# Performance work log

Hardware: AMD Instinct MI355X
Metric: run time of the kernel (lower is better)

Reference implementation:

```python
import jax, jax.numpy as jnp
import numpy as np

N = 100000
D = 512


def setup_inputs() -> dict:
    key = jax.random.key(0)
    k1, k2 = jax.random.split(key)
    features = jax.random.normal(k1, (N, D), dtype=jnp.float32)
    attn_w = jax.random.normal(k2, (D,), dtype=jnp.float32)
    attn_b = jnp.zeros((1,), dtype=jnp.float32)
    return {"features": features, "attn_w": attn_w, "attn_b": attn_b, "k": 4}


def reference(features, attn_w, attn_b, k):
    # features: [N, D]; sliding-window (half-width k, truncated at edges) mean
    n = features.shape[0]
    zero = jnp.zeros((1, features.shape[1]), dtype=features.dtype)
    cs = jnp.concatenate([zero, jnp.cumsum(features, axis=0)], axis=0)  # [N+1, D]
    i = jnp.arange(n)
    lo = jnp.maximum(i - k, 0)          # inclusive window start
    hi = jnp.minimum(i + k, n - 1)      # inclusive window end
    win_sum = cs[hi + 1] - cs[lo]       # [N, D]
    count = (hi - lo + 1).astype(features.dtype)[:, None]
    agg = win_sum / count               # [N, D] windowed means
    scores = agg @ attn_w + attn_b[0]   # [N]
    w = jax.nn.softmax(scores, axis=0)  # [N]
    bag = w @ agg                       # [D]
    return bag, w
```

## Files before the change

### kernel.cpp

```cpp
#include <hip/hip_runtime.h>
#include <math.h>

#define D 512
#define OWN 128
#define HALOA 8

__device__ __forceinline__ float dot4(float4 a, float4 b) {
    return a.x*b.x + a.y*b.y + a.z*b.z + a.w*b.w;
}

__global__ __launch_bounds__(256) void k_ab(
    const float* __restrict__ f, const float* __restrict__ w,
    const float* __restrict__ bptr, const int* __restrict__ kptr,
    float* __restrict__ e_out, float* __restrict__ psum,
    float* __restrict__ partial, int n)
{
    __shared__ float dots[OWN + 2 * HALOA];
    __shared__ float e_sh[OWN + 2 * HALOA];
    __shared__ float uu_sh[OWN];
    __shared__ float sm[4];
    int lane = threadIdx.x & 63;
    int wid  = threadIdx.x >> 6;
    int t    = threadIdx.x;
    int g0   = blockIdx.x * OWN - HALOA;

    const float4* wr = (const float4*)w;
    float4 b0 = wr[lane], b1 = wr[lane + 64];

    for (int lr = wid; lr < OWN + 2 * HALOA; lr += 4) {
        int row = g0 + lr;
        bool v = (row >= 0) && (row < n);
        const float4* fr = (const float4*)(f + (size_t)(v ? row : 0) * D);
        float4 a0 = fr[lane], a1 = fr[lane + 64];
        float s = dot4(a0, b0) + dot4(a1, b1);
        #pragma unroll
        for (int off = 32; off; off >>= 1) s += __shfl_down(s, off);
        if (lane == 0) dots[lr] = v ? s : 0.f;
    }
    __syncthreads();

    int k = *kptr;
    float bias = bptr[0];

    float e_reg = 0.f;
    if (t < OWN + 2 * HALOA) {
        int i = g0 + t;
        if (t >= HALOA - k && t < HALOA + OWN + k && i >= 0 && i < n) {
            int lo = max(i - k, 0), hi = min(i + k, n - 1);
            float s = 0.f;
            for (int q = lo; q <= hi; ++q) s += dots[q - g0];
            e_reg = __expf(s / (float)(hi - lo + 1) + bias);
        }
        e_sh[t] = e_reg;
    }
    __syncthreads();

    float pv = (t >= HALOA && t < HALOA + OWN) ? e_reg : 0.f;
    #pragma unroll
    for (int off = 32; off; off >>= 1) pv += __shfl_down(pv, off);
    if (lane == 0) sm[wid] = pv;
    __syncthreads();
    if (t == 0) psum[blockIdx.x] = sm[0] + sm[1] + sm[2] + sm[3];

    if (t < OWN) {
        int j = blockIdx.x * OWN + t;
        float acc = 0.f;
        if (j < n) {
            e_out[j] = e_sh[t + HALOA];
            int lo = max(j - k, 0), hi = min(j + k, n - 1);
            for (int i = lo; i <= hi; ++i) {
                int li = max(i - k, 0), hh = min(i + k, n - 1);
                acc += e_sh[i - g0] * __builtin_amdgcn_rcpf((float)(hh - li + 1));
            }
        }
        uu_sh[t] = acc;
    }
    __syncthreads();

    if (t < 128) {
        int j0 = blockIdx.x * OWN;
        int j1 = min(j0 + OWN, n);
        float4 acc0 = make_float4(0.f,0.f,0.f,0.f);
        float4 acc1 = make_float4(0.f,0.f,0.f,0.f);
        float4 acc2 = make_float4(0.f,0.f,0.f,0.f);
        float4 acc3 = make_float4(0.f,0.f,0.f,0.f);
        int j = j0;
        for (; j + 4 <= j1; j += 4) {
            int lr = j - j0;
            float u0 = uu_sh[lr], u1 = uu_sh[lr+1], u2 = uu_sh[lr+2], u3 = uu_sh[lr+3];
            float4 v0 = ((const float4*)(f + (size_t)(j  ) * D))[t];
            float4 v1 = ((const float4*)(f + (size_t)(j+1) * D))[t];
            float4 v2 = ((const float4*)(f + (size_t)(j+2) * D))[t];
            float4 v3 = ((const float4*)(f + (size_t)(j+3) * D))[t];
            acc0.x += u0*v0.x; acc0.y += u0*v0.y; acc0.z += u0*v0.z; acc0.w += u0*v0.w;
            acc1.x += u1*v1.x; acc1.y += u1*v1.y; acc1.z += u1*v1.z; acc1.w += u1*v1.w;
            acc2.x += u2*v2.x; acc2.y += u2*v2.y; acc2.z += u2*v2.z; acc2.w += u2*v2.w;
            acc3.x += u3*v3.x; acc3.y += u3*v3.y; acc3.z += u3*v3.z; acc3.w += u3*v3.w;
        }
        for (; j < j1; ++j) {
            float uj = uu_sh[j - j0];
            float4 v = ((const float4*)(f + (size_t)j * D))[t];
            acc0.x += uj*v.x; acc0.y += uj*v.y; acc0.z += uj*v.z; acc0.w += uj*v.w;
        }
        float4 a;
        a.x = (acc0.x + acc1.x) + (acc2.x + acc3.x);
        a.y = (acc0.y + acc1.y) + (acc2.y + acc3.y);
        a.z = (acc0.z + acc1.z) + (acc2.z + acc3.z);
        a.w = (acc0.w + acc1.w) + (acc2.w + acc3.w);
        ((float4*)(partial + (size_t)blockIdx.x * D))[t] = a;
    }
}

__global__ void k_final(const float* __restrict__ partial, const float* __restrict__ psum,
                        int nbp, int nbs, const float* __restrict__ e,
                        float* __restrict__ bag, float* __restrict__ w_out, int n) {
    __shared__ float sm[4];
    __shared__ float ginv;
    int lane = threadIdx.x & 63, wid = threadIdx.x >> 6;

    float s = 0.f;
    for (int idx = threadIdx.x; idx < nbs; idx += 256) s += psum[idx];
    #pragma unroll
    for (int off = 32; off; off >>= 1) s += __shfl_down(s, off);
    if (lane == 0) sm[wid] = s;
    __syncthreads();
    if (threadIdx.x == 0)
        ginv = 1.f / (sm[0] + sm[1] + sm[2] + sm[3]);
    __syncthreads();
    float inv = ginv;

    if (blockIdx.x < 32) {
        int c = blockIdx.x * 16 + (threadIdx.x & 15);
        int r = threadIdx.x >> 4;
        float acc = 0.f;
        for (int b = r; b < nbp; b += 16) acc += partial[(size_t)b * D + c];
        __shared__ float sred[256];
        sred[threadIdx.x] = acc;
        __syncthreads();
        if (threadIdx.x < 16) {
            float tt = 0.f;
            #pragma unroll
            for (int q = 0; q < 16; ++q) tt += sred[q * 16 + threadIdx.x];
            bag[blockIdx.x * 16 + threadIdx.x] = tt * inv;
        }
    }

    for (int j = blockIdx.x * 256 + threadIdx.x; j < n; j += gridDim.x * 256)
        w_out[j] = e[j] * inv;
}

extern "C" void kernel_launch(void* const* d_in, const int* in_sizes, int n_in,
                              void* d_out, int out_size, void* d_ws, size_t ws_size,
                              hipStream_t stream) {
    const float* f  = (const float*)d_in[0];
    const float* aw = (const float*)d_in[1];
    const float* ab = (const float*)d_in[2];
    const int*   kp = (const int*)d_in[3];
    int n = in_sizes[0] / D;

    float* bag   = (float*)d_out;
    float* w_out = (float*)d_out + D;

    int nbA = (n + OWN - 1) / OWN;
    int nb2 = (n + 255) / 256;

    float* wsf     = (float*)d_ws;
    float* e       = wsf;
    float* psum    = wsf + n;
    size_t poff    = (((size_t)n + (size_t)nbA) + 31) & ~(size_t)31;
    float* partial = wsf + poff;

    k_ab   <<<nbA, 256, 0, stream>>>(f, aw, ab, kp, e, psum, partial, n);
    k_final<<<nb2, 256, 0, stream>>>(partial, psum, nbA, nbA, e, bag, w_out, n);
}
```

Baseline: 81.98 us.

## Fuse final reduction into main kernel via atomic last-blocks completion counter

Merges the second reduction kernel into the main kernel. Each block bumps an atomic counter when it finishes, and the last 32 blocks to arrive spin until every block is done. Those blocks then reduce the partial sums, write bag, and normalise w. This removes a second kernel launch and its dependency gap, but adds a memset, a spin-wait, and a final phase that runs on only 32 blocks.

```diff
diff --git a/kernel.cpp b/kernel.cpp
--- a/kernel.cpp
+++ b/kernel.cpp
@@ -4,21 +4,26 @@
 #define D 512
 #define OWN 128
 #define HALOA 8
+#define NFIN 32
 
 __device__ __forceinline__ float dot4(float4 a, float4 b) {
     return a.x*b.x + a.y*b.y + a.z*b.z + a.w*b.w;
 }
 
-__global__ __launch_bounds__(256) void k_ab(
+__global__ __launch_bounds__(256) void k_all(
     const float* __restrict__ f, const float* __restrict__ w,
     const float* __restrict__ bptr, const int* __restrict__ kptr,
     float* __restrict__ e_out, float* __restrict__ psum,
-    float* __restrict__ partial, int n)
+    float* __restrict__ partial, float* __restrict__ bag,
+    float* __restrict__ w_out, int* cnt, int n, int nbA)
 {
     __shared__ float dots[OWN + 2 * HALOA];
     __shared__ float e_sh[OWN + 2 * HALOA];
     __shared__ float uu_sh[OWN];
     __shared__ float sm[4];
+    __shared__ float ginv;
+    __shared__ int   s_old;
+    __shared__ float sred[256];
     int lane = threadIdx.x & 63;
     int wid  = threadIdx.x >> 6;
     int t    = threadIdx.x;
@@ -109,44 +114,53 @@
         a.w = (acc0.w + acc1.w) + (acc2.w + acc3.w);
         ((float4*)(partial + (size_t)blockIdx.x * D))[t] = a;
     }
-}
 
-__global__ void k_final(const float* __restrict__ partial, const float* __restrict__ psum,
-                        int nbp, int nbs, const float* __restrict__ e,
-                        float* __restrict__ bag, float* __restrict__ w_out, int n) {
-    __shared__ float sm[4];
-    __shared__ float ginv;
-    int lane = threadIdx.x & 63, wid = threadIdx.x >> 6;
+    __syncthreads();
+    if (t == 0) {
+        __threadfence();
+        s_old = atomicAdd(cnt, 1);
+    }
+    __syncthreads();
+    int old = s_old;
+    if (old < nbA - NFIN) return;
+    int li = old - (nbA - NFIN);
+
+    if (t == 0) {
+        while (__hip_atomic_load(cnt, __ATOMIC_ACQUIRE, __HIP_MEMORY_SCOPE_AGENT) < nbA)
+            __builtin_amdgcn_s_sleep(2);
+        __threadfence();
+    }
+    __syncthreads();
 
     float s = 0.f;
-    for (int idx = threadIdx.x; idx < nbs; idx += 256) s += psum[idx];
+    for (int idx = t; idx < nbA; idx += 256) s += psum[idx];
     #pragma unroll
     for (int off = 32; off; off >>= 1) s += __shfl_down(s, off);
     if (lane == 0) sm[wid] = s;
     __syncthreads();
-    if (threadIdx.x == 0)
-        ginv = 1.f / (sm[0] + sm[1] + sm[2] + sm[3]);
+    if (t == 0) ginv = 1.f / (sm[0] + sm[1] + sm[2] + sm[3]);
     __syncthreads();
     float inv = ginv;
 
-    if (blockIdx.x < 32) {
-        int c = blockIdx.x * 16 + (threadIdx.x & 15);
-        int r = threadIdx.x >> 4;
+    {
+        int c = li * 16 + (t & 15);
+        int r = t >> 4;
         float acc = 0.f;
-        for (int b = r; b < nbp; b += 16) acc += partial[(size_t)b * D + c];
-        __shared__ float sred[256];
-        sred[threadIdx.x] = acc;
+        for (int b = r; b < nbA; b += 16) acc += partial[(size_t)b * D + c];
+        sred[t] = acc;
         __syncthreads();
-        if (threadIdx.x < 16) {
+        if (t < 16) {
             float tt = 0.f;
             #pragma unroll
-            for (int q = 0; q < 16; ++q) tt += sred[q * 16 + threadIdx.x];
-            bag[blockIdx.x * 16 + threadIdx.x] = tt * inv;
+            for (int q = 0; q < 16; ++q) tt += sred[q * 16 + t];
+            bag[li * 16 + t] = tt * inv;
         }
     }
 
-    for (int j = blockIdx.x * 256 + threadIdx.x; j < n; j += gridDim.x * 256)
-        w_out[j] = e[j] * inv;
+    int per = (n + NFIN - 1) / NFIN;
+    int jend = min(li * per + per, n);
+    for (int j = li * per + t; j < jend; j += 256)
+        w_out[j] = e_out[j] * inv;
 }
 
 extern "C" void kernel_launch(void* const* d_in, const int* in_sizes, int n_in,
@@ -162,14 +176,15 @@
     float* w_out = (float*)d_out + D;
 
     int nbA = (n + OWN - 1) / OWN;
-    int nb2 = (n + 255) / 256;
 
+    int*   cnt     = (int*)d_ws;
     float* wsf     = (float*)d_ws;
-    float* e       = wsf;
-    float* psum    = wsf + n;
-    size_t poff    = (((size_t)n + (size_t)nbA) + 31) & ~(size_t)31;
+    float* e       = wsf + 16;
+    float* psum    = e + n;
+    size_t poff    = ((16 + (size_t)n + (size_t)nbA) + 31) & ~(size_t)31;
     float* partial = wsf + poff;
 
-    k_ab   <<<nbA, 256, 0, stream>>>(f, aw, ab, kp, e, psum, partial, n);
-    k_final<<<nb2, 256, 0, stream>>>(partial, psum, nbA, nbA, e, bag, w_out, n);
+    hipMemsetAsync(cnt, 0, 64, stream);
+    k_all<<<nbA, 256, 0, stream>>>(f, aw, ab, kp, e, psum, partial,
+                                   bag, w_out, cnt, n, nbA);
 }
```

New measurement: 113.9 us. +38.9%, slower.

## Split row-dot computation into a separate kernel before windowed bag pass

Applied to the files above, without the earlier changes.

Moves the per-row dot product with the attention weight out of the fused block kernel into its own kernel, k_dot, which writes one scalar per row to workspace. The main kernel then loads precomputed dots for its tile plus a widened halo of 16 instead of recomputing dots for halo rows. This removes redundant halo dot work and gives the bag pass a simpler prologue. In exchange, the 200 MB feature matrix is read twice, once per kernel, with an extra launch; it may partly hit in cache but likely adds memory traffic.

```diff
diff --git a/kernel.cpp b/kernel.cpp
--- a/kernel.cpp
+++ b/kernel.cpp
@@ -3,39 +3,48 @@
 
 #define D 512
 #define OWN 128
-#define HALOA 8
+#define HX 16
 
 __device__ __forceinline__ float dot4(float4 a, float4 b) {
     return a.x*b.x + a.y*b.y + a.z*b.z + a.w*b.w;
 }
 
-__global__ __launch_bounds__(256) void k_ab(
-    const float* __restrict__ f, const float* __restrict__ w,
+__global__ void k_dot(const float* __restrict__ f, const float* __restrict__ w,
+                      float* __restrict__ dot, int n) {
+    int wave = threadIdx.x >> 6;
+    int lane = threadIdx.x & 63;
+    int row  = blockIdx.x * 4 + wave;
+    if (row >= n) return;
+    const float4* fr = (const float4*)(f + (size_t)row * D);
+    const float4* wr = (const float4*)w;
+    float4 a0 = fr[lane],      b0 = wr[lane];
+    float4 a1 = fr[lane + 64], b1 = wr[lane + 64];
+    float s = a0.x*b0.x + a0.y*b0.y + a0.z*b0.z + a0.w*b0.w
+            + a1.x*b1.x + a1.y*b1.y + a1.z*b1.z + a1.w*b1.w;
+    #pragma unroll
+    for (int off = 32; off; off >>= 1) s += __shfl_down(s, off);
+    if (lane == 0) dot[row] = s;
+}
+
+__global__ __launch_bounds__(256) void k_ebag(
+    const float* __restrict__ f, const float* __restrict__ dot,
     const float* __restrict__ bptr, const int* __restrict__ kptr,
     float* __restrict__ e_out, float* __restrict__ psum,
     float* __restrict__ partial, int n)
 {
-    __shared__ float dots[OWN + 2 * HALOA];
-    __shared__ float e_sh[OWN + 2 * HALOA];
+    __shared__ float dots_sh[OWN + 2 * HX];
+    __shared__ float e_sh[OWN + 2 * HX];
     __shared__ float uu_sh[OWN];
     __shared__ float sm[4];
     int lane = threadIdx.x & 63;
     int wid  = threadIdx.x >> 6;
     int t    = threadIdx.x;
-    int g0   = blockIdx.x * OWN - HALOA;
+    int j0   = blockIdx.x * OWN;
+    int gd0  = j0 - HX;
 
-    const float4* wr = (const float4*)w;
-    float4 b0 = wr[lane], b1 = wr[lane + 64];
-
-    for (int lr = wid; lr < OWN + 2 * HALOA; lr += 4) {
-        int row = g0 + lr;
-        bool v = (row >= 0) && (row < n);
-        const float4* fr = (const float4*)(f + (size_t)(v ? row : 0) * D);
-        float4 a0 = fr[lane], a1 = fr[lane + 64];
-        float s = dot4(a0, b0) + dot4(a1, b1);
-        #pragma unroll
-        for (int off = 32; off; off >>= 1) s += __shfl_down(s, off);
-        if (lane == 0) dots[lr] = v ? s : 0.f;
+    if (t < OWN + 2 * HX) {
+        int gq = gd0 + t;
+        dots_sh[t] = (gq >= 0 && gq < n) ? dot[gq] : 0.f;
     }
     __syncthreads();
 
@@ -43,19 +52,19 @@
     float bias = bptr[0];
 
     float e_reg = 0.f;
-    if (t < OWN + 2 * HALOA) {
-        int i = g0 + t;
-        if (t >= HALOA - k && t < HALOA + OWN + k && i >= 0 && i < n) {
+    if (t < OWN + 2 * HX) {
+        int i = gd0 + t;
+        if (t >= HX - k && t < HX + OWN + k && i >= 0 && i < n) {
             int lo = max(i - k, 0), hi = min(i + k, n - 1);
             float s = 0.f;
-            for (int q = lo; q <= hi; ++q) s += dots[q - g0];
+            for (int q = lo; q <= hi; ++q) s += dots_sh[q - gd0];
             e_reg = __expf(s / (float)(hi - lo + 1) + bias);
         }
         e_sh[t] = e_reg;
     }
     __syncthreads();
 
-    float pv = (t >= HALOA && t < HALOA + OWN) ? e_reg : 0.f;
+    float pv = (t < OWN) ? e_sh[t + HX] : 0.f;
     #pragma unroll
     for (int off = 32; off; off >>= 1) pv += __shfl_down(pv, off);
     if (lane == 0) sm[wid] = pv;
@@ -63,14 +72,14 @@
     if (t == 0) psum[blockIdx.x] = sm[0] + sm[1] + sm[2] + sm[3];
 
     if (t < OWN) {
-        int j = blockIdx.x * OWN + t;
+        int j = j0 + t;
         float acc = 0.f;
         if (j < n) {
-            e_out[j] = e_sh[t + HALOA];
+            e_out[j] = e_sh[t + HX];
             int lo = max(j - k, 0), hi = min(j + k, n - 1);
             for (int i = lo; i <= hi; ++i) {
                 int li = max(i - k, 0), hh = min(i + k, n - 1);
-                acc += e_sh[i - g0] * __builtin_amdgcn_rcpf((float)(hh - li + 1));
+                acc += e_sh[i - gd0] * __builtin_amdgcn_rcpf((float)(hh - li + 1));
             }
         }
         uu_sh[t] = acc;
@@ -78,7 +87,6 @@
     __syncthreads();
 
     if (t < 128) {
-        int j0 = blockIdx.x * OWN;
         int j1 = min(j0 + OWN, n);
         float4 acc0 = make_float4(0.f,0.f,0.f,0.f);
         float4 acc1 = make_float4(0.f,0.f,0.f,0.f);
@@ -165,11 +173,13 @@
     int nb2 = (n + 255) / 256;
 
     float* wsf     = (float*)d_ws;
-    float* e       = wsf;
-    float* psum    = wsf + n;
-    size_t poff    = (((size_t)n + (size_t)nbA) + 31) & ~(size_t)31;
+    float* dot     = wsf;
+    float* e       = wsf + n;
+    float* psum    = wsf + 2 * (size_t)n;
+    size_t poff    = ((2 * (size_t)n + (size_t)nbA) + 31) & ~(size_t)31;
     float* partial = wsf + poff;
 
-    k_ab   <<<nbA, 256, 0, stream>>>(f, aw, ab, kp, e, psum, partial, n);
+    k_dot  <<<(n + 3) / 4, 256, 0, stream>>>(f, aw, dot, n);
+    k_ebag <<<nbA, 256, 0, stream>>>(f, dot, ab, kp, e, psum, partial, n);
     k_final<<<nb2, 256, 0, stream>>>(partial, psum, nbA, nbA, e, bag, w_out, n);
 }
```

Measured after the change: 83.06 us. No clear change (+1.3%).
